# Optimization experiments

Hardware: AMD Instinct MI355X
Metric: run time of the kernel (lower is better)

## Reference

```python
import math
import jax, jax.numpy as jnp
import numpy as np

EMBED = 1024
HIDDEN = 1024
HEADS = 16


def setup_inputs() -> dict:
    key = jax.random.key(0)
    ks = jax.random.split(key, 9)
    B, S = 1, 4096
    s = 1.0 / math.sqrt(EMBED)
    return {
        "x": jax.random.normal(ks[0], (B, S, EMBED), dtype=jnp.float32),
        "Wq": jax.random.normal(ks[1], (EMBED, HIDDEN), dtype=jnp.float32) * s,
        "bq": jnp.zeros((HIDDEN,), dtype=jnp.float32),
        "Wk": jax.random.normal(ks[2], (EMBED, HIDDEN), dtype=jnp.float32) * s,
        "bk": jnp.zeros((HIDDEN,), dtype=jnp.float32),
        "Wv": jax.random.normal(ks[3], (EMBED, HIDDEN), dtype=jnp.float32) * s,
        "bv": jnp.zeros((HIDDEN,), dtype=jnp.float32),
        "Wo": jax.random.normal(ks[4], (EMBED, HIDDEN), dtype=jnp.float32) * s,
        "bo": jnp.zeros((HIDDEN,), dtype=jnp.float32),
    }


def reference(x, Wq, bq, Wk, bk, Wv, bv, Wo, bo):
    B, S, _ = x.shape
    Hd = HIDDEN // HEADS
    # projections: [B,S,hidden] -> [B,H,S,hd]
    def split_heads(t):
        return t.reshape(B, S, HEADS, Hd).transpose(0, 2, 1, 3)
    q = split_heads(x @ Wq + bq)
    k = split_heads(x @ Wk + bk)
    v = split_heads(x @ Wv + bv)
    scale = 1.0 / math.sqrt(EMBED / HEADS)
    scores = jnp.einsum("bhqd,bhkd->bhqk", q, k) * scale  # [B,H,S,S]
    attn = jax.nn.softmax(scores, axis=-1)
    ctx = jnp.einsum("bhqk,bhkd->bhqd", attn, v)
    ctx = ctx.transpose(0, 2, 1, 3).reshape(B, S, HIDDEN)
    return ctx @ Wo + bo
```

## Files before the change

kernel.cpp:

```cpp
#include <hip/hip_runtime.h>
#include <hip/hip_bf16.h>
#include <math.h>

typedef __bf16 bf16;
typedef bf16  bf16x2 __attribute__((ext_vector_type(2)));
typedef bf16  bf16x4 __attribute__((ext_vector_type(4)));
typedef bf16  bf16x8 __attribute__((ext_vector_type(8)));
typedef float f32x4  __attribute__((ext_vector_type(4)));
typedef float f32x16 __attribute__((ext_vector_type(16)));
typedef unsigned uint4v __attribute__((ext_vector_type(4)));

#define MFMA16(a, b, c) __builtin_amdgcn_mfma_f32_16x16x32_bf16((a), (b), (c), 0, 0, 0)
#define MFMA32(a, b, c) __builtin_amdgcn_mfma_f32_32x32x16_bf16((a), (b), (c), 0, 0, 0)

static constexpr int S  = 4096;
static constexpr int E  = 1024;
static constexpr int NH = 16;
static constexpr int HD = 64;

__device__ __forceinline__ void gload16(const bf16* g, bf16* l) {
    __builtin_amdgcn_global_load_lds(
        (const __attribute__((address_space(1))) void*)g,
        (__attribute__((address_space(3))) void*)l, 16, 0, 0);
}

__device__ __forceinline__ int xcd_swizzle(int nwg) {
    const int orig = blockIdx.x + gridDim.x * blockIdx.y;
    return (orig & 7) * (nwg >> 3) + (orig >> 3);
}

__global__ void convert_f32_bf16(const float* __restrict__ in, bf16* __restrict__ out, int n) {
    int i = (blockIdx.x * blockDim.x + threadIdx.x) * 8;
    if (i < n) {
        float4 v0 = *(const float4*)(in + i);
        float4 v1 = *(const float4*)(in + i + 4);
        bf16x8 o = { (bf16)v0.x, (bf16)v0.y, (bf16)v0.z, (bf16)v0.w,
                     (bf16)v1.x, (bf16)v1.y, (bf16)v1.z, (bf16)v1.w };
        *(bf16x8*)(out + i) = o;
    }
}

__global__ void transpose_w(const float* __restrict__ W0, const float* __restrict__ W1,
                            const float* __restrict__ W2, const float* __restrict__ W3,
                            bf16* __restrict__ T0, bf16* __restrict__ T1,
                            bf16* __restrict__ T2, bf16* __restrict__ T3) {
    const float* W; bf16* T;
    switch (blockIdx.z) {
        case 0: W = W0; T = T0; break;
        case 1: W = W1; T = T1; break;
        case 2: W = W2; T = T2; break;
        default: W = W3; T = T3; break;
    }
    __shared__ float tile[64][65];
    int k0 = blockIdx.x * 64, n0 = blockIdx.y * 64;
    #pragma unroll
    for (int i = 0; i < 16; i++) {
        int idx = threadIdx.x + i * 256;
        int r = idx >> 6, c = idx & 63;
        tile[r][c] = W[(k0 + r) * E + n0 + c];
    }
    __syncthreads();
    #pragma unroll
    for (int i = 0; i < 8; i++) {
        int idx = threadIdx.x + i * 256;
        int r = idx >> 5, c2 = (idx & 31) * 2;
        bf16x2 v = { (bf16)tile[c2][r], (bf16)tile[c2 + 1][r] };
        *(bf16x2*)(T + (n0 + r) * E + k0 + c2) = v;
    }
}

__global__ __launch_bounds__(512) void gemm256_qkv(const bf16* __restrict__ A,
                                                   const bf16* __restrict__ BT,
                                                   const float* __restrict__ b0,
                                                   const float* __restrict__ b1,
                                                   const float* __restrict__ b2,
                                                   bf16* __restrict__ outQ,
                                                   bf16* __restrict__ outK,
                                                   bf16* __restrict__ outV,
                                                   float qscale) {
    extern __shared__ char lds[];
    const int tid = threadIdx.x, lane = tid & 63, w = tid >> 6;
    const int wm = w >> 2, wn = w & 3;
    const int sbid = xcd_swizzle(16 * 12);
    const int m0 = (sbid % 16) * 256, n0 = (sbid / 16) * 256;
    const int ln = lane & 15, g = lane >> 4;
    const int swz = (ln & 7) << 4;

    const int sr   = w * 16 + (lane >> 3);
    const int scol = ((lane & 7) ^ ((lane >> 3) & 7)) * 8;
    const bf16* Ag = A  + (size_t)(m0 + sr) * E + scol;
    const bf16* Bg = BT + (size_t)(n0 + sr) * E + scol;

    auto stageT = [&](int buf, int t) {
        const int kc = t * 64;
        #pragma unroll
        for (int hh = 0; hh < 2; hh++)
            #pragma unroll
            for (int j = 0; j < 2; j++)
                gload16(Ag + (size_t)(hh * 128 + j * 8) * E + kc,
                        (bf16*)(lds + (buf * 2 + hh) * 16384 + (w * 16 + j * 8) * 128));
        #pragma unroll
        for (int hh = 0; hh < 2; hh++)
            #pragma unroll
            for (int j = 0; j < 2; j++)
                gload16(Bg + (size_t)(hh * 128 + j * 8) * E + kc,
                        (bf16*)(lds + 65536 + (buf * 2 + hh) * 16384 + (w * 16 + j * 8) * 128));
    };

    f32x4 acc[8][4] = {};
    const int brow = (wn & 1) * 64;
    constexpr int NT = E / 64;

    stageT(0, 0);
    for (int i = 0; i < NT; i++) {
        const int cur = i & 1;
        if (i + 1 < NT) {
            stageT(cur ^ 1, i + 1);
            asm volatile("s_waitcnt vmcnt(8)" ::: "memory");
        } else {
            asm volatile("s_waitcnt vmcnt(0)" ::: "memory");
        }
        __builtin_amdgcn_s_barrier();
        __builtin_amdgcn_sched_barrier(0);

        const char* Ab = lds + (cur * 2 + wm) * 16384;
        const char* Bb = lds + 65536 + (cur * 2 + (wn >> 1)) * 16384;
        #pragma unroll
        for (int kh = 0; kh < 2; kh++) {
            const int cb = kh * 64 + g * 16;
            bf16x8 bfr[4];
            #pragma unroll
            for (int bj = 0; bj < 4; bj++)
                bfr[bj] = *(const bf16x8*)(Bb + (brow + bj * 16 + ln) * 128 + (cb ^ swz));
            __builtin_amdgcn_s_setprio(1);
            #pragma unroll
            for (int mi = 0; mi < 8; mi++) {
                bf16x8 af = *(const bf16x8*)(Ab + (mi * 16 + ln) * 128 + (cb ^ swz));
                #pragma unroll
                for (int bj = 0; bj < 4; bj++)
                    acc[mi][bj] = MFMA16(af, bfr[bj], acc[mi][bj]);
            }
            __builtin_amdgcn_s_setprio(0);
        }
        asm volatile("s_waitcnt lgkmcnt(0)" ::: "memory");
        __builtin_amdgcn_sched_barrier(0);
        __builtin_amdgcn_s_barrier();
    }

    const int proj = n0 >> 10;
    const float* bias = proj == 0 ? b0 : (proj == 1 ? b1 : b2);
    bf16* outp = proj == 0 ? outQ : (proj == 1 ? outK : outV);
    const float osc = proj == 0 ? qscale : 1.0f;
    if (proj < 2) {
        #pragma unroll
        for (int bj = 0; bj < 4; bj++) {
            const int nn = (n0 + wn * 64 + bj * 16 + ln) & 1023;
            const int hh = nn >> 6, dd = nn & 63;
            const float bb = bias[nn];
            #pragma unroll
            for (int mi = 0; mi < 8; mi++) {
                const int m = m0 + wm * 128 + mi * 16 + g * 4;
                #pragma unroll
                for (int r = 0; r < 4; r++)
                    outp[((size_t)hh * S + m + r) * HD + dd] = (bf16)((acc[mi][bj][r] + bb) * osc);
            }
        }
    } else {
        #pragma unroll
        for (int bj = 0; bj < 4; bj++) {
            const int nn = (n0 + wn * 64 + bj * 16 + ln) & 1023;
            const float bb = bias[nn];
            #pragma unroll
            for (int mi = 0; mi < 8; mi++) {
                const int m = m0 + wm * 128 + mi * 16 + g * 4;
                bf16x4 vv = { (bf16)(acc[mi][bj][0] + bb), (bf16)(acc[mi][bj][1] + bb),
                              (bf16)(acc[mi][bj][2] + bb), (bf16)(acc[mi][bj][3] + bb) };
                *(bf16x4*)(outp + (size_t)nn * S + m) = vv;
            }
        }
    }
}

__global__ __launch_bounds__(256) void gemm_o(const bf16* __restrict__ A,
                                              const bf16* __restrict__ BT,
                                              const float* __restrict__ bias,
                                              float* __restrict__ outp) {
    __shared__ __align__(16) bf16 Als[2][128 * 32];
    __shared__ __align__(16) bf16 Bls[2][128 * 32];
    const int tid = threadIdx.x, lane = tid & 63, w = tid >> 6;
    const int wm = w >> 1, wn = w & 1;
    const int sbid = xcd_swizzle(32 * 8);
    const int m0 = (sbid % 32) * 128, n0 = (sbid / 32) * 128;
    const int ln = lane & 15, g = lane >> 4;

    const bf16* Ag = A  + (size_t)(m0 + w * 32 + (lane >> 2)) * E + (lane & 3) * 8;
    const bf16* Bg = BT + (size_t)(n0 + w * 32 + (lane >> 2)) * E + (lane & 3) * 8;

    auto stage = [&](int buf, int kt) {
        #pragma unroll
        for (int j = 0; j < 2; j++) {
            gload16(Ag + j * 16 * E + kt, (bf16*)((char*)&Als[buf][0] + w * 2048 + j * 1024));
            gload16(Bg + j * 16 * E + kt, (bf16*)((char*)&Bls[buf][0] + w * 2048 + j * 1024));
        }
    };

    f32x4 acc[4][4] = {};
    stage(0, 0);
    int cur = 0;
    for (int kt = 0; kt < E; kt += 32, cur ^= 1) {
        if (kt + 32 < E) {
            stage(cur ^ 1, kt + 32);
            asm volatile("s_waitcnt vmcnt(4)" ::: "memory");
        } else {
            asm volatile("s_waitcnt vmcnt(0)" ::: "memory");
        }
        __builtin_amdgcn_s_barrier();
        __builtin_amdgcn_sched_barrier(0);

        bf16x8 af[4], bfr[4];
        #pragma unroll
        for (int i = 0; i < 4; i++) {
            af[i]  = *(const bf16x8*)(&Als[cur][0] + (wm * 64 + i * 16 + ln) * 32 + g * 8);
            bfr[i] = *(const bf16x8*)(&Bls[cur][0] + (wn * 64 + i * 16 + ln) * 32 + g * 8);
        }
        __builtin_amdgcn_s_setprio(1);
        #pragma unroll
        for (int mi = 0; mi < 4; mi++)
            #pragma unroll
            for (int bj = 0; bj < 4; bj++)
                acc[mi][bj] = MFMA16(af[mi], bfr[bj], acc[mi][bj]);
        __builtin_amdgcn_s_setprio(0);
        asm volatile("s_waitcnt lgkmcnt(0)" ::: "memory");
        __builtin_amdgcn_sched_barrier(0);
        __builtin_amdgcn_s_barrier();
    }

    #pragma unroll
    for (int bj = 0; bj < 4; bj++) {
        const int n = n0 + wn * 64 + bj * 16 + ln;
        const float bb = bias[n];
        #pragma unroll
        for (int mi = 0; mi < 4; mi++) {
            const int m = m0 + wm * 64 + mi * 16 + g * 4;
            #pragma unroll
            for (int r = 0; r < 4; r++)
                outp[(size_t)(m + r) * E + n] = acc[mi][bj][r] + bb;
        }
    }
}

__global__ __launch_bounds__(512) void flash_attn5(const bf16* __restrict__ Qh,
                                                   const bf16* __restrict__ Kh,
                                                   const bf16* __restrict__ Vt,
                                                   bf16* __restrict__ ctx) {
    __shared__ __align__(16) char smem[65536];
    const int tid = threadIdx.x, lane = tid & 63, w = tid >> 6;
    const int w4 = w & 3, kvh = w >> 2;
    const int sbid = xcd_swizzle(32 * NH);
    const int qb = sbid % 32, h = sbid / 32;
    const int l31 = lane & 31, h5 = lane >> 5;
    const int q_global = qb * 128 + w4 * 32 + l31;

    const bf16* Qbase = Qh + ((size_t)h * S + q_global) * HD;
    bf16x8 qf[4];
    #pragma unroll
    for (int t = 0; t < 4; t++) qf[t] = *(const bf16x8*)(Qbase + t * 16 + h5 * 8);

    const int srow = w4 * 16 + (lane >> 3);
    const int scol = ((lane & 7) ^ (lane >> 3)) * 8;
    const int swz  = (lane & 7) << 4;

    char* const Kb0 = smem + kvh * 16384;
    char* const Vb0 = smem + 32768 + kvh * 16384;

    auto stage = [&](int buf, int kv) {
        #pragma unroll
        for (int j = 0; j < 2; j++) {
            gload16(Kh + ((size_t)h * S + kv + srow + j * 8) * HD + scol,
                    (bf16*)(Kb0 + buf * 8192 + w4 * 2048 + j * 1024));
            gload16(Vt + ((size_t)(h * HD + srow + j * 8)) * S + kv + scol,
                    (bf16*)(Vb0 + buf * 8192 + w4 * 2048 + j * 1024));
        }
    };

    auto exppack = [&](const f32x16& s, bf16x8& pa, bf16x8& pc, float& rs) {
        unsigned d[8];
        #pragma unroll
        for (int i = 0; i < 8; i++) {
            float e0 = __builtin_amdgcn_exp2f(s[2 * i]);
            float e1 = __builtin_amdgcn_exp2f(s[2 * i + 1]);
            rs += e0 + e1;
            asm("v_cvt_pk_bf16_f32 %0, %1, %2" : "=v"(d[i]) : "v"(e0), "v"(e1));
        }
        asm volatile("v_permlane32_swap_b32 %0, %1" : "+v"(d[0]), "+v"(d[2]));
        asm volatile("v_permlane32_swap_b32 %0, %1" : "+v"(d[1]), "+v"(d[3]));
        asm volatile("v_permlane32_swap_b32 %0, %1" : "+v"(d[4]), "+v"(d[6]));
        asm volatile("v_permlane32_swap_b32 %0, %1" : "+v"(d[5]), "+v"(d[7]));
        uint4v fa = { d[0], d[1], d[2], d[3] }, fb = { d[4], d[5], d[6], d[7] };
        pa = __builtin_bit_cast(bf16x8, fa);
        pc = __builtin_bit_cast(bf16x8, fb);
    };

    f32x16 o0 = {}, o1 = {};
    float l_i = 0.f;
    const int kv0 = kvh * (S / 2);
    constexpr int NT = S / 128;

    stage(0, kv0);
    for (int t = 0; t < NT; t++) {
        const int cur = t & 1;
        __syncthreads();
        if (t + 1 < NT) stage(cur ^ 1, kv0 + (t + 1) * 64);

        const char* Kb = Kb0 + cur * 8192;
        const char* Vb = Vb0 + cur * 8192;

        f32x16 s0 = {}, s1 = {};
        __builtin_amdgcn_s_setprio(1);
        #pragma unroll
        for (int t4 = 0; t4 < 4; t4++) {
            const int cb = (t4 * 32 + h5 * 16) ^ swz;
            bf16x8 k0 = *(const bf16x8*)(Kb + l31 * 128 + cb);
            bf16x8 k1 = *(const bf16x8*)(Kb + (32 + l31) * 128 + cb);
            s0 = MFMA32(k0, qf[t4], s0);
            s1 = MFMA32(k1, qf[t4], s1);
        }
        __builtin_amdgcn_s_setprio(0);

        bf16x8 pb[4];
        float rs = 0.f;
        exppack(s0, pb[0], pb[1], rs);
        exppack(s1, pb[2], pb[3], rs);
        l_i += rs;

        __builtin_amdgcn_s_setprio(1);
        #pragma unroll
        for (int ks = 0; ks < 4; ks++) {
            const int cb = (ks * 32 + h5 * 16) ^ swz;
            bf16x8 va  = *(const bf16x8*)(Vb + l31 * 128 + cb);
            bf16x8 vb2 = *(const bf16x8*)(Vb + (32 + l31) * 128 + cb);
            o0 = MFMA32(va, pb[ks], o0);
            o1 = MFMA32(vb2, pb[ks], o1);
        }
        __builtin_amdgcn_s_setprio(0);
    }

    __syncthreads();
    float* const lr  = (float*)(smem + 32768);
    float* const orr = (float*)smem + w4 * 2048;
    if (w >= 4) {
        lr[w4 * 64 + lane] = l_i;
        #pragma unroll
        for (int r = 0; r < 16; r++) orr[r * 64 + lane]        = o0[r];
        #pragma unroll
        for (int r = 0; r < 16; r++) orr[(16 + r) * 64 + lane] = o1[r];
    }
    __syncthreads();
    if (w < 4) {
        l_i += lr[w4 * 64 + lane];
        #pragma unroll
        for (int r = 0; r < 16; r++) o0[r] += orr[r * 64 + lane];
        #pragma unroll
        for (int r = 0; r < 16; r++) o1[r] += orr[(16 + r) * 64 + lane];
        l_i += __shfl_xor(l_i, 32);
        const float inv = 1.f / l_i;
        bf16* cbase = ctx + (size_t)q_global * E + h * HD;
        #pragma unroll
        for (int dg = 0; dg < 2; dg++) {
            const f32x16& o = dg ? o1 : o0;
            #pragma unroll
            for (int rq = 0; rq < 4; rq++) {
                bf16x4 ov = { (bf16)(o[rq * 4 + 0] * inv), (bf16)(o[rq * 4 + 1] * inv),
                              (bf16)(o[rq * 4 + 2] * inv), (bf16)(o[rq * 4 + 3] * inv) };
                *(bf16x4*)(cbase + dg * 32 + rq * 8 + h5 * 4) = ov;
            }
        }
    }
}

extern "C" void kernel_launch(void* const* d_in, const int* in_sizes, int n_in,
                              void* d_out, int out_size, void* d_ws, size_t ws_size,
                              hipStream_t stream) {
    const float* x  = (const float*)d_in[0];
    const float* Wq = (const float*)d_in[1];
    const float* bq = (const float*)d_in[2];
    const float* Wk = (const float*)d_in[3];
    const float* bk = (const float*)d_in[4];
    const float* Wv = (const float*)d_in[5];
    const float* bv = (const float*)d_in[6];
    const float* Wo = (const float*)d_in[7];
    const float* bo = (const float*)d_in[8];

    char* ws = (char*)d_ws;
    const size_t MB = 1u << 20;
    bf16* xb   = (bf16*)(ws + 0 * MB);
    bf16* Wcat = (bf16*)(ws + 8 * MB);
    bf16* tq   = Wcat;
    bf16* tk   = Wcat + 1024 * 1024;
    bf16* tv   = Wcat + 2048 * 1024;
    bf16* to   = (bf16*)(ws + 14 * MB);
    bf16* Qh   = (bf16*)(ws + 16 * MB);
    bf16* Kh   = (bf16*)(ws + 24 * MB);
    bf16* Vt   = (bf16*)(ws + 32 * MB);
    bf16* ctx  = (bf16*)(ws + 40 * MB);

    const float qscale = 0.125f * 1.44269504088896f;

    convert_f32_bf16<<<dim3(S * E / 2048), 256, 0, stream>>>(x, xb, S * E);
    transpose_w<<<dim3(16, 16, 4), 256, 0, stream>>>(Wq, Wk, Wv, Wo, tq, tk, tv, to);

    gemm256_qkv<<<dim3(S / 256, 3072 / 256), 512, 131072, stream>>>(
        xb, Wcat, bq, bk, bv, Qh, Kh, Vt, qscale);

    flash_attn5<<<dim3(S / 128, NH), 512, 0, stream>>>(Qh, Kh, Vt, ctx);

    gemm_o<<<dim3(S / 128, E / 128), 256, 0, stream>>>(ctx, to, bo, (float*)d_out);
}
```

Before: 148.8 us.

## Give each attention wave 64 queries and drop XCD block swizzling

The flash attention kernel now runs 4 waves per block instead of 8. Each wave handles 64 query rows as two 32-row MFMA groups, so every K and V fragment read from LDS feeds two MFMAs and LDS read traffic per FLOP is halved. Each wave also stages twice as many rows per tile. The cost is more accumulator registers per wave (four 16-float O tiles plus two S tiles), which may lower occupancy, and there are fewer waves per block to hide latency. XCD-aware block remapping is also removed from the GEMMs and attention in favour of plain blockIdx mapping, which may change L2 locality.

```diff
diff --git a/kernel.cpp b/kernel.cpp
--- a/kernel.cpp
+++ b/kernel.cpp
@@ -22,11 +22,6 @@
     __builtin_amdgcn_global_load_lds(
         (const __attribute__((address_space(1))) void*)g,
         (__attribute__((address_space(3))) void*)l, 16, 0, 0);
-}
-
-__device__ __forceinline__ int xcd_swizzle(int nwg) {
-    const int orig = blockIdx.x + gridDim.x * blockIdx.y;
-    return (orig & 7) * (nwg >> 3) + (orig >> 3);
 }
 
 __global__ void convert_f32_bf16(const float* __restrict__ in, bf16* __restrict__ out, int n) {
@@ -81,8 +76,7 @@
     extern __shared__ char lds[];
     const int tid = threadIdx.x, lane = tid & 63, w = tid >> 6;
     const int wm = w >> 2, wn = w & 3;
-    const int sbid = xcd_swizzle(16 * 12);
-    const int m0 = (sbid % 16) * 256, n0 = (sbid / 16) * 256;
+    const int m0 = blockIdx.x * 256, n0 = blockIdx.y * 256;
     const int ln = lane & 15, g = lane >> 4;
     const int swz = (ln & 7) << 4;
 
@@ -189,8 +183,7 @@
     __shared__ __align__(16) bf16 Bls[2][128 * 32];
     const int tid = threadIdx.x, lane = tid & 63, w = tid >> 6;
     const int wm = w >> 1, wn = w & 1;
-    const int sbid = xcd_swizzle(32 * 8);
-    const int m0 = (sbid % 32) * 128, n0 = (sbid / 32) * 128;
+    const int m0 = blockIdx.x * 128, n0 = blockIdx.y * 128;
     const int ln = lane & 15, g = lane >> 4;
 
     const bf16* Ag = A  + (size_t)(m0 + w * 32 + (lane >> 2)) * E + (lane & 3) * 8;
@@ -249,25 +242,26 @@
     }
 }
 
-__global__ __launch_bounds__(512) void flash_attn5(const bf16* __restrict__ Qh,
+__global__ __launch_bounds__(256) void flash_attn9(const bf16* __restrict__ Qh,
                                                    const bf16* __restrict__ Kh,
                                                    const bf16* __restrict__ Vt,
                                                    bf16* __restrict__ ctx) {
     __shared__ __align__(16) char smem[65536];
     const int tid = threadIdx.x, lane = tid & 63, w = tid >> 6;
-    const int w4 = w & 3, kvh = w >> 2;
-    const int sbid = xcd_swizzle(32 * NH);
-    const int qb = sbid % 32, h = sbid / 32;
+    const int qsub = w & 1, kvh = w >> 1;
+    const int h = blockIdx.y, qb = blockIdx.x;
     const int l31 = lane & 31, h5 = lane >> 5;
-    const int q_global = qb * 128 + w4 * 32 + l31;
-
-    const bf16* Qbase = Qh + ((size_t)h * S + q_global) * HD;
-    bf16x8 qf[4];
+
+    const bf16* Qb0 = Qh + ((size_t)h * S + qb * 128 + qsub * 64 + l31) * HD;
+    bf16x8 qf0[4], qf1[4];
     #pragma unroll
-    for (int t = 0; t < 4; t++) qf[t] = *(const bf16x8*)(Qbase + t * 16 + h5 * 8);
-
-    const int srow = w4 * 16 + (lane >> 3);
-    const int scol = ((lane & 7) ^ (lane >> 3)) * 8;
+    for (int t = 0; t < 4; t++) {
+        qf0[t] = *(const bf16x8*)(Qb0 + t * 16 + h5 * 8);
+        qf1[t] = *(const bf16x8*)(Qb0 + 32 * HD + t * 16 + h5 * 8);
+    }
+
+    const int srow = qsub * 32 + (lane >> 3);
+    const int scol = ((lane & 7) ^ ((lane >> 3) & 7)) * 8;
     const int swz  = (lane & 7) << 4;
 
     char* const Kb0 = smem + kvh * 16384;
@@ -275,11 +269,11 @@
 
     auto stage = [&](int buf, int kv) {
         #pragma unroll
-        for (int j = 0; j < 2; j++) {
+        for (int j = 0; j < 4; j++) {
             gload16(Kh + ((size_t)h * S + kv + srow + j * 8) * HD + scol,
-                    (bf16*)(Kb0 + buf * 8192 + w4 * 2048 + j * 1024));
+                    (bf16*)(Kb0 + buf * 8192 + qsub * 4096 + j * 1024));
             gload16(Vt + ((size_t)(h * HD + srow + j * 8)) * S + kv + scol,
-                    (bf16*)(Vb0 + buf * 8192 + w4 * 2048 + j * 1024));
+                    (bf16*)(Vb0 + buf * 8192 + qsub * 4096 + j * 1024));
         }
     };
 
@@ -301,8 +295,8 @@
         pc = __builtin_bit_cast(bf16x8, fb);
     };
 
-    f32x16 o0 = {}, o1 = {};
-    float l_i = 0.f;
+    f32x16 o00 = {}, o01 = {}, o10 = {}, o11 = {};
+    float l0 = 0.f, l1 = 0.f;
     const int kv0 = kvh * (S / 2);
     constexpr int NT = S / 128;
 
@@ -315,64 +309,87 @@
         const char* Kb = Kb0 + cur * 8192;
         const char* Vb = Vb0 + cur * 8192;
 
-        f32x16 s0 = {}, s1 = {};
-        __builtin_amdgcn_s_setprio(1);
-        #pragma unroll
-        for (int t4 = 0; t4 < 4; t4++) {
-            const int cb = (t4 * 32 + h5 * 16) ^ swz;
-            bf16x8 k0 = *(const bf16x8*)(Kb + l31 * 128 + cb);
-            bf16x8 k1 = *(const bf16x8*)(Kb + (32 + l31) * 128 + cb);
-            s0 = MFMA32(k0, qf[t4], s0);
-            s1 = MFMA32(k1, qf[t4], s1);
-        }
-        __builtin_amdgcn_s_setprio(0);
-
-        bf16x8 pb[4];
-        float rs = 0.f;
-        exppack(s0, pb[0], pb[1], rs);
-        exppack(s1, pb[2], pb[3], rs);
-        l_i += rs;
-
-        __builtin_amdgcn_s_setprio(1);
-        #pragma unroll
-        for (int ks = 0; ks < 4; ks++) {
-            const int cb = (ks * 32 + h5 * 16) ^ swz;
-            bf16x8 va  = *(const bf16x8*)(Vb + l31 * 128 + cb);
-            bf16x8 vb2 = *(const bf16x8*)(Vb + (32 + l31) * 128 + cb);
-            o0 = MFMA32(va, pb[ks], o0);
-            o1 = MFMA32(vb2, pb[ks], o1);
-        }
-        __builtin_amdgcn_s_setprio(0);
+        #pragma unroll
+        for (int khalf = 0; khalf < 2; khalf++) {
+            f32x16 s0 = {}, s1 = {};
+            __builtin_amdgcn_s_setprio(1);
+            #pragma unroll
+            for (int t4 = 0; t4 < 4; t4++) {
+                const int cb = (t4 * 32 + h5 * 16) ^ swz;
+                bf16x8 kk = *(const bf16x8*)(Kb + (khalf * 32 + l31) * 128 + cb);
+                s0 = MFMA32(kk, qf0[t4], s0);
+                s1 = MFMA32(kk, qf1[t4], s1);
+            }
+            __builtin_amdgcn_s_setprio(0);
+
+            bf16x8 p00, p01, p10, p11;
+            exppack(s0, p00, p01, l0);
+            exppack(s1, p10, p11, l1);
+
+            __builtin_amdgcn_s_setprio(1);
+            #pragma unroll
+            for (int sub = 0; sub < 2; sub++) {
+                const int cbv = ((khalf * 2 + sub) * 32 + h5 * 16) ^ swz;
+                const bf16x8 pA = sub ? p01 : p00;
+                const bf16x8 pB = sub ? p11 : p10;
+                bf16x8 va0 = *(const bf16x8*)(Vb + l31 * 128 + cbv);
+                bf16x8 va1 = *(const bf16x8*)(Vb + (32 + l31) * 128 + cbv);
+                o00 = MFMA32(va0, pA, o00);
+                o01 = MFMA32(va0, pB, o01);
+                o10 = MFMA32(va1, pA, o10);
+                o11 = MFMA32(va1, pB, o11);
+            }
+            __builtin_amdgcn_s_setprio(0);
+        }
     }
 
     __syncthreads();
-    float* const lr  = (float*)(smem + 32768);
-    float* const orr = (float*)smem + w4 * 2048;
-    if (w >= 4) {
-        lr[w4 * 64 + lane] = l_i;
-        #pragma unroll
-        for (int r = 0; r < 16; r++) orr[r * 64 + lane]        = o0[r];
-        #pragma unroll
-        for (int r = 0; r < 16; r++) orr[(16 + r) * 64 + lane] = o1[r];
+    float* const Ob = (float*)smem;
+    float* const Lb = (float*)(smem + 32768);
+    if (kvh == 1) {
+        float* Or = Ob + qsub * 4096;
+        #pragma unroll
+        for (int r = 0; r < 16; r++) Or[r * 64 + lane]        = o00[r];
+        #pragma unroll
+        for (int r = 0; r < 16; r++) Or[(16 + r) * 64 + lane] = o01[r];
+        #pragma unroll
+        for (int r = 0; r < 16; r++) Or[(32 + r) * 64 + lane] = o10[r];
+        #pragma unroll
+        for (int r = 0; r < 16; r++) Or[(48 + r) * 64 + lane] = o11[r];
+        Lb[qsub * 128 + lane]      = l0;
+        Lb[qsub * 128 + 64 + lane] = l1;
     }
     __syncthreads();
-    if (w < 4) {
-        l_i += lr[w4 * 64 + lane];
-        #pragma unroll
-        for (int r = 0; r < 16; r++) o0[r] += orr[r * 64 + lane];
-        #pragma unroll
-        for (int r = 0; r < 16; r++) o1[r] += orr[(16 + r) * 64 + lane];
-        l_i += __shfl_xor(l_i, 32);
-        const float inv = 1.f / l_i;
-        bf16* cbase = ctx + (size_t)q_global * E + h * HD;
+    if (kvh == 0) {
+        float* Or = Ob + qsub * 4096;
+        #pragma unroll
+        for (int r = 0; r < 16; r++) o00[r] += Or[r * 64 + lane];
+        #pragma unroll
+        for (int r = 0; r < 16; r++) o01[r] += Or[(16 + r) * 64 + lane];
+        #pragma unroll
+        for (int r = 0; r < 16; r++) o10[r] += Or[(32 + r) * 64 + lane];
+        #pragma unroll
+        for (int r = 0; r < 16; r++) o11[r] += Or[(48 + r) * 64 + lane];
+        l0 += Lb[qsub * 128 + lane];
+        l1 += Lb[qsub * 128 + 64 + lane];
+        l0 += __shfl_xor(l0, 32);
+        l1 += __shfl_xor(l1, 32);
+        const float inv0 = 1.f / l0, inv1 = 1.f / l1;
+
+        bf16* c0 = ctx + (size_t)(qb * 128 + qsub * 64 + l31) * E + h * HD;
+        bf16* c1 = c0 + (size_t)32 * E;
         #pragma unroll
         for (int dg = 0; dg < 2; dg++) {
-            const f32x16& o = dg ? o1 : o0;
+            const f32x16& oa = dg ? o10 : o00;
+            const f32x16& ob = dg ? o11 : o01;
             #pragma unroll
             for (int rq = 0; rq < 4; rq++) {
-                bf16x4 ov = { (bf16)(o[rq * 4 + 0] * inv), (bf16)(o[rq * 4 + 1] * inv),
-                              (bf16)(o[rq * 4 + 2] * inv), (bf16)(o[rq * 4 + 3] * inv) };
-                *(bf16x4*)(cbase + dg * 32 + rq * 8 + h5 * 4) = ov;
+                bf16x4 va = { (bf16)(oa[rq * 4 + 0] * inv0), (bf16)(oa[rq * 4 + 1] * inv0),
+                              (bf16)(oa[rq * 4 + 2] * inv0), (bf16)(oa[rq * 4 + 3] * inv0) };
+                bf16x4 vb = { (bf16)(ob[rq * 4 + 0] * inv1), (bf16)(ob[rq * 4 + 1] * inv1),
+                              (bf16)(ob[rq * 4 + 2] * inv1), (bf16)(ob[rq * 4 + 3] * inv1) };
+                *(bf16x4*)(c0 + dg * 32 + rq * 8 + h5 * 4) = va;
+                *(bf16x4*)(c1 + dg * 32 + rq * 8 + h5 * 4) = vb;
             }
         }
     }
@@ -412,7 +429,7 @@
     gemm256_qkv<<<dim3(S / 256, 3072 / 256), 512, 131072, stream>>>(
         xb, Wcat, bq, bk, bv, Qh, Kh, Vt, qscale);
 
-    flash_attn5<<<dim3(S / 128, NH), 512, 0, stream>>>(Qh, Kh, Vt, ctx);
+    flash_attn9<<<dim3(S / 128, NH), 256, 0, stream>>>(Qh, Kh, Vt, ctx);
 
     gemm_o<<<dim3(S / 128, E / 128), 256, 0, stream>>>(ctx, to, bo, (float*)d_out);
 }
```

New measurement: 156.3 us. 5.0% more time.
